# Kernel optimization log

Hardware: AMD Instinct MI355X
Metric: run time of the kernel (lower is better)

## Reference

```python
import jax, jax.numpy as jnp
import numpy as np

D_MODEL = 1024
N_HEADS = 16
HEAD_DIM = D_MODEL // N_HEADS


def setup_inputs() -> dict:
    key = jax.random.key(0)
    k1, k2, k3 = jax.random.split(key, 3)
    B, T, C = 4, 2048, D_MODEL
    x = jax.random.normal(k1, (B, T, C), dtype=jnp.float32)
    # torch Linear weight is (out,in); store as (in,out) so y = x @ W
    w_qkv = jax.random.normal(k2, (C, 3 * C), dtype=jnp.float32) * (1.0 / np.sqrt(C))
    w_proj = jax.random.normal(k3, (C, C), dtype=jnp.float32) * (1.0 / np.sqrt(C))
    return {"x": x, "w_qkv": w_qkv, "w_proj": w_proj}


def reference(x, w_qkv, w_proj):
    B, T, C = x.shape
    H, Dh = N_HEADS, HEAD_DIM
    qkv = x @ w_qkv                        # (B,T,3C)
    q, k, v = jnp.split(qkv, 3, axis=-1)
    def heads(t):
        return t.reshape(B, T, H, Dh).transpose(0, 2, 1, 3)  # (B,H,T,Dh)
    q, k, v = heads(q), heads(k), heads(v)
    scores = jnp.einsum('bhqd,bhkd->bhqk', q, k) / np.sqrt(Dh).astype(np.float32)
    causal = jnp.tril(jnp.ones((T, T), dtype=bool))
    scores = jnp.where(causal, scores, -jnp.inf)
    attn = jax.nn.softmax(scores, axis=-1)
    y = jnp.einsum('bhqk,bhkd->bhqd', attn, v)  # (B,H,T,Dh)
    y = y.transpose(0, 2, 1, 3).reshape(B, T, C)
    return y @ w_proj
```

## Files before the change

### kernel.cpp

```cpp
#include <hip/hip_runtime.h>

#define SEQ_T 2048
#define NBATCH 4
#define CDIM 1024
#define NHEAD 16
#define MROWS 8192
#define QKVC 3072

typedef unsigned short u16;
typedef __bf16 bf16x8 __attribute__((ext_vector_type(8)));
typedef float f32x4 __attribute__((ext_vector_type(4)));
typedef unsigned short u16x8 __attribute__((ext_vector_type(8)));
typedef unsigned uint32x4 __attribute__((ext_vector_type(4)));

__device__ __forceinline__ u16 f32_to_bf16(float f) {
  union { float f; unsigned int u; } v; v.f = f;
  unsigned int u = v.u;
  unsigned int r = ((u >> 16) & 1u) + 0x7fffu;
  return (u16)((u + r) >> 16);
}

__device__ __forceinline__ void gload_lds16(const u16* g, u16* l) {
  __builtin_amdgcn_global_load_lds(
      (const __attribute__((address_space(1))) void*)g,
      (__attribute__((address_space(3))) void*)l, 16, 0, 0);
}


__global__ __launch_bounds__(256) void cast_block_kernel(const float* __restrict__ in,
                                                         u16* __restrict__ out) {
  const int i = blockIdx.x * 256 + threadIdx.x;
  const int kg = i & 127;
  const int row = i >> 7;
  const float4 v0 = ((const float4*)in)[i * 2];
  const float4 v1 = ((const float4*)in)[i * 2 + 1];
  union { u16 u[8]; bf16x8 b; } o;
  o.u[0] = f32_to_bf16(v0.x); o.u[1] = f32_to_bf16(v0.y);
  o.u[2] = f32_to_bf16(v0.z); o.u[3] = f32_to_bf16(v0.w);
  o.u[4] = f32_to_bf16(v1.x); o.u[5] = f32_to_bf16(v1.y);
  o.u[6] = f32_to_bf16(v1.z); o.u[7] = f32_to_bf16(v1.w);
  const int tile = (row >> 4) * 32 + (kg >> 2);
  const int lane = (row & 15) + ((kg & 3) << 4);
  *(bf16x8*)(out + (size_t)tile * 512 + lane * 8) = o.b;
}

__global__ void transpose_cast_block_kernel(const float* __restrict__ in,
                                            u16* __restrict__ out) {
  __shared__ float tile[32][33];
  const int c0 = blockIdx.x * 32, r0 = blockIdx.y * 32;
  const int tx = threadIdx.x, ty = threadIdx.y;
  #pragma unroll
  for (int i = 0; i < 32; i += 8)
    tile[ty + i][tx] = in[(size_t)(r0 + ty + i) * QKVC + c0 + tx];
  __syncthreads();
  const int t = ty * 32 + tx;
  if (t < 128) {
    const int cc = t & 31, kgq = t >> 5;
    union { u16 u[8]; bf16x8 b; } o;
    #pragma unroll
    for (int j = 0; j < 8; ++j) o.u[j] = f32_to_bf16(tile[kgq * 8 + j][cc]);
    const int rowN = c0 + cc;
    const int tileI = (rowN >> 4) * 32 + (r0 >> 5);
    const int lane = (rowN & 15) + (kgq << 4);
    *(bf16x8*)(out + (size_t)tileI * 512 + lane * 8) = o.b;
  }
}

__global__ void transpose_cast_kernel(const float* __restrict__ in, u16* __restrict__ out,
                                      int R, int Cc) {
  __shared__ float tile[32][33];
  int c0 = blockIdx.x * 32, r0 = blockIdx.y * 32;
  int tx = threadIdx.x, ty = threadIdx.y;
  #pragma unroll
  for (int i = 0; i < 32; i += 8)
    tile[ty + i][tx] = in[(size_t)(r0 + ty + i) * Cc + c0 + tx];
  __syncthreads();
  #pragma unroll
  for (int i = 0; i < 32; i += 8)
    out[(size_t)(c0 + ty + i) * R + r0 + tx] = f32_to_bf16(tile[tx][ty + i]);
}

__global__ __launch_bounds__(256, 3)
void gemm1_kernel(const u16* __restrict__ Ab, const u16* __restrict__ Bb,
                  u16* __restrict__ Qb, u16* __restrict__ Kc, u16* __restrict__ Vc) {
  __shared__ u16 lds[24576];
  const int tid = threadIdx.x;
  const int lane = tid & 63, w = tid >> 6;
  const int wm = w >> 1, wn = w & 1;
  const int l15 = lane & 15, lhi = lane >> 4;
  const int row0 = blockIdx.x * 128, col0 = blockIdx.y * 128;
  const int rt0 = row0 >> 4, ct0 = col0 >> 4;

  const u16* aT = Ab + (size_t)(rt0 + w * 2) * 16384 + lane * 8;
  const u16* bT = Bb + (size_t)(ct0 + w * 2) * 16384 + lane * 8;

  f32x4 acc[4][4] = {};

#define SA(S) (lds + (S) * 4096)
#define SB(S) (lds + 12288 + (S) * 4096)
#define STAGE(KT, S)                                                            \
  {                                                                             \
    gload_lds16(aT + (size_t)(KT) * 512,         SA(S) + (w * 2) * 512);        \
    gload_lds16(aT + 16384 + (size_t)(KT) * 512, SA(S) + (w * 2 + 1) * 512);    \
    gload_lds16(bT + (size_t)(KT) * 512,         SB(S) + (w * 2) * 512);        \
    gload_lds16(bT + 16384 + (size_t)(KT) * 512, SB(S) + (w * 2 + 1) * 512);    \
  }
#define COMPUTE(S)                                                              \
  {                                                                             \
    bf16x8 af[4], bf[4];                                                        \
    _Pragma("unroll") for (int mi = 0; mi < 4; ++mi)                            \
      af[mi] = *(const bf16x8*)(SA(S) + (wm * 4 + mi) * 512 + lane * 8);        \
    _Pragma("unroll") for (int ni = 0; ni < 4; ++ni)                            \
      bf[ni] = *(const bf16x8*)(SB(S) + (wn * 4 + ni) * 512 + lane * 8);        \
    __builtin_amdgcn_s_setprio(1);                                              \
    _Pragma("unroll") for (int mi = 0; mi < 4; ++mi)                            \
      _Pragma("unroll") for (int ni = 0; ni < 4; ++ni)                          \
        acc[mi][ni] = __builtin_amdgcn_mfma_f32_16x16x32_bf16(af[mi], bf[ni],   \
                                                              acc[mi][ni], 0, 0, 0); \
    __builtin_amdgcn_s_setprio(0);                                              \
  }
#define WAITBAR4                                                                \
  asm volatile("s_waitcnt vmcnt(4)" ::: "memory");                              \
  __builtin_amdgcn_sched_barrier(0);                                            \
  __builtin_amdgcn_s_barrier();

  STAGE(0, 0);
  STAGE(1, 1);
  WAITBAR4;

  #pragma unroll 1
  for (int kt = 0; kt < 30; kt += 3) {
    STAGE(kt + 2, 2); COMPUTE(0); WAITBAR4;
    STAGE(kt + 3, 0); COMPUTE(1); WAITBAR4;
    STAGE(kt + 4, 1); COMPUTE(2); WAITBAR4;
  }
  COMPUTE(0);
  asm volatile("s_waitcnt vmcnt(0)" ::: "memory");
  __builtin_amdgcn_sched_barrier(0);
  __builtin_amdgcn_s_barrier();
  COMPUTE(1);
#undef STAGE
#undef COMPUTE
#undef WAITBAR4
#undef SA
#undef SB

  const int region = col0 >> 10;
  if (region == 0) {
    #pragma unroll
    for (int mt = 0; mt < 4; ++mt)
      #pragma unroll
      for (int nt = 0; nt < 4; ++nt)
        #pragma unroll
        for (int r = 0; r < 4; ++r) {
          const int rr = row0 + wm * 64 + mt * 16 + lhi * 4 + r;
          const int cc = col0 + wn * 64 + nt * 16 + l15;
          Qb[(size_t)rr * CDIM + cc] = f32_to_bf16(acc[mt][nt][r] * 0.18033688011f);
        }
  } else {
    __syncthreads();
    if (region == 1) {
      #pragma unroll
      for (int mt = 0; mt < 4; ++mt)
        #pragma unroll
        for (int nt = 0; nt < 4; ++nt)
          #pragma unroll
          for (int r = 0; r < 4; ++r) {
            const int sidx = (wn * 4 + wm * 2 + (mt >> 1)) * 2048
                           + ((mt & 1) * 2 + (nt >> 1)) * 512
                           + ((nt & 1) * 2 + (l15 >> 3)) * 128
                           + (lhi * 4 + r) * 8 + (l15 & 7);
            lds[sidx] = f32_to_bf16(acc[mt][nt][r]);
          }
    } else {
      #pragma unroll
      for (int mt = 0; mt < 4; ++mt)
        #pragma unroll
        for (int nt = 0; nt < 4; ++nt)
          #pragma unroll
          for (int r = 0; r < 4; ++r) {
            const int sidx = (wn * 4 + wm * 2 + (mt >> 1)) * 2048
                           + nt * 512
                           + ((mt & 1) * 2 + (lhi >> 1)) * 128
                           + l15 * 8 + (lhi & 1) * 4 + r;
            lds[sidx] = f32_to_bf16(acc[mt][nt][r]);
          }
    }
    __syncthreads();
    u16* dstB = (region == 1) ? Kc : Vc;
    const int bb = row0 >> 11;
    const int kv0b = (row0 & 2047) >> 5;
    const int hbase = (col0 & 1023) >> 6;
    #pragma unroll
    for (int hh = 0; hh < 2; ++hh) {
      u16* dst = dstB + (size_t)(bb * 16 + hbase + hh) * 131072 + (size_t)kv0b * 2048;
      const u16* src = lds + hh * 8192;
      #pragma unroll
      for (int c = 0; c < 4; ++c) {
        const int o = (c * 256 + tid) * 8;
        *(uint32x4*)(dst + o) = *(const uint32x4*)(src + o);
      }
    }
  }
}

__global__ __launch_bounds__(256, 3)
void gemm2_kernel(const u16* __restrict__ A, const u16* __restrict__ Bt,
                  float* __restrict__ C, int N, int K) {
  __shared__ u16 sA[3][4096];
  __shared__ u16 sB[3][4096];
  const int tid = threadIdx.x;
  const int lane = tid & 63, w = tid >> 6;
  const int wm = w >> 1, wn = w & 1;
  const int l15 = lane & 15, lhi = lane >> 4;
  const int row0 = blockIdx.x * 128, col0 = blockIdx.y * 128;

  const int oln  = ((lane & 3) - (lane >> 2)) & 3;
  const int srow = w * 32 + (lane >> 2);
  const u16* aS = A  + (size_t)(row0 + srow) * K + oln * 8;
  const u16* bS = Bt + (size_t)(col0 + srow) * K + oln * 8;
  const int stD = w * 1024;
  const int rdA = (wm * 64 + l15) * 32 + ((lhi + l15) & 3) * 8;
  const int rdB = (wn * 64 + l15) * 32 + ((lhi + l15) & 3) * 8;

  f32x4 acc[4][4] = {};

#define STAGE(KT, S)                                                            \
  {                                                                             \
    const size_t ko = (size_t)(KT) * 32;                                        \
    gload_lds16(aS + ko,          &sA[S][stD]);                                 \
    gload_lds16(aS + ko + 16 * K, &sA[S][stD + 512]);                           \
    gload_lds16(bS + ko,          &sB[S][stD]);                                 \
    gload_lds16(bS + ko + 16 * K, &sB[S][stD + 512]);                           \
  }
#define COMPUTE(S)                                                              \
  {                                                                             \
    bf16x8 af[4], bf[4];                                                        \
    _Pragma("unroll") for (int mi = 0; mi < 4; ++mi)                            \
      af[mi] = *(const bf16x8*)&sA[S][rdA + mi * 512];                          \
    _Pragma("unroll") for (int ni = 0; ni < 4; ++ni)                            \
      bf[ni] = *(const bf16x8*)&sB[S][rdB + ni * 512];                          \
    __builtin_amdgcn_s_setprio(1);                                              \
    _Pragma("unroll") for (int mi = 0; mi < 4; ++mi)                            \
      _Pragma("unroll") for (int ni = 0; ni < 4; ++ni)                          \
        acc[mi][ni] = __builtin_amdgcn_mfma_f32_16x16x32_bf16(af[mi], bf[ni],   \
                                                              acc[mi][ni], 0, 0, 0); \
    __builtin_amdgcn_s_setprio(0);                                              \
  }
#define WAITBAR4                                                                \
  asm volatile("s_waitcnt vmcnt(4)" ::: "memory");                              \
  __builtin_amdgcn_sched_barrier(0);                                            \
  __builtin_amdgcn_s_barrier();

  STAGE(0, 0);
  STAGE(1, 1);
  WAITBAR4;

  #pragma unroll 1
  for (int kt = 0; kt < 30; kt += 3) {
    STAGE(kt + 2, 2); COMPUTE(0); WAITBAR4;
    STAGE(kt + 3, 0); COMPUTE(1); WAITBAR4;
    STAGE(kt + 4, 1); COMPUTE(2); WAITBAR4;
  }
  COMPUTE(0);
  asm volatile("s_waitcnt vmcnt(0)" ::: "memory");
  __builtin_amdgcn_sched_barrier(0);
  __builtin_amdgcn_s_barrier();
  COMPUTE(1);
#undef STAGE
#undef COMPUTE
#undef WAITBAR4

  #pragma unroll
  for (int mt = 0; mt < 4; ++mt)
    #pragma unroll
    for (int nt = 0; nt < 4; ++nt)
      #pragma unroll
      for (int r = 0; r < 4; ++r) {
        const int rr = row0 + wm * 64 + mt * 16 + lhi * 4 + r;
        const int cc = col0 + wn * 64 + nt * 16 + l15;
        C[(size_t)rr * N + cc] = acc[mt][nt][r];
      }
}

template <bool DOMASK>
__device__ __forceinline__ void attn_step(const bf16x8 (&qf)[2],
                                          const bf16x8 (&kf)[2][2],
                                          const bf16x8 (&vb)[4],
                                          const bf16x8 ones,
                                          f32x4 (&acc)[4], f32x4& acc1,
                                          int l15, int lhi, int kv0, int qg) {
  f32x4 st[2];
  #pragma unroll
  for (int t = 0; t < 2; ++t) {
    f32x4 z = {0.f, 0.f, 0.f, 0.f};
    z = __builtin_amdgcn_mfma_f32_16x16x32_bf16(kf[t][0], qf[0], z, 0, 0, 0);
    z = __builtin_amdgcn_mfma_f32_16x16x32_bf16(kf[t][1], qf[1], z, 0, 0, 0);
    st[t] = z;
  }
  #pragma unroll
  for (int t = 0; t < 2; ++t)
    #pragma unroll
    for (int r = 0; r < 4; ++r) {
      float sv = st[t][r];
      if (DOMASK) {
        const int kvg = kv0 + t * 16 + lhi * 4 + r;
        sv = (kvg > qg) ? -__builtin_inff() : sv;
      }
      st[t][r] = exp2f(sv);
    }
  unsigned c00, c01, c10, c11;
  asm("v_cvt_pk_bf16_f32 %0, %1, %2" : "=v"(c00) : "v"(st[0][0]), "v"(st[0][1]));
  asm("v_cvt_pk_bf16_f32 %0, %1, %2" : "=v"(c01) : "v"(st[0][2]), "v"(st[0][3]));
  asm("v_cvt_pk_bf16_f32 %0, %1, %2" : "=v"(c10) : "v"(st[1][0]), "v"(st[1][1]));
  asm("v_cvt_pk_bf16_f32 %0, %1, %2" : "=v"(c11) : "v"(st[1][2]), "v"(st[1][3]));
  asm("v_permlane32_swap_b32 %0, %1" : "+v"(c00), "+v"(c10));
  asm("v_permlane32_swap_b32 %0, %1" : "+v"(c01), "+v"(c11));
  asm("v_permlane16_swap_b32 %0, %1" : "+v"(c00), "+v"(c10));
  asm("v_permlane16_swap_b32 %0, %1" : "+v"(c01), "+v"(c11));
  uint32x4 pw; pw[0] = c00; pw[1] = c01; pw[2] = c10; pw[3] = c11;
  const bf16x8 pa = __builtin_bit_cast(bf16x8, pw);
  #pragma unroll
  for (int d = 0; d < 4; ++d)
    acc[d] = __builtin_amdgcn_mfma_f32_16x16x32_bf16(pa, vb[d], acc[d], 0, 0, 0);
  acc1 = __builtin_amdgcn_mfma_f32_16x16x32_bf16(pa, ones, acc1, 0, 0, 0);
}

__global__ __launch_bounds__(256, 4) void attn_kernel(const u16* __restrict__ Qb,
                                                      const u16* __restrict__ Kc,
                                                      const u16* __restrict__ Vc,
                                                      u16* __restrict__ Y) {
  __shared__ u16 Kl[2][2048];
  __shared__ u16 Vl[2][2048];
  const int tid = threadIdx.x, lane = tid & 63, wid = tid >> 6;
  const int l15 = lane & 15, lhi = lane >> 4;
  const int id = blockIdx.x;
  const int xcd = id & 7, k = (id >> 3) & 15, hi3 = id >> 7;
  const int bh = hi3 * 8 + xcd;
  const int b = bh >> 4, h = bh & 15;
  const int pa = k * 4 + wid;
  const int qA0 = pa * 16, qB0 = (127 - pa) * 16;
  const int nchA = pa / 2 + 1, nchB = (127 - pa) / 2 + 1;
  const int ncmax = (127 - k * 4) / 2 + 1;
  const u16* Qp  = Qb + (size_t)b * SEQ_T * CDIM + h * 64;
  const u16* KcC = Kc + (size_t)bh * 131072;
  const u16* VcC = Vc + (size_t)bh * 131072;

  u16x8 ou;
  #pragma unroll
  for (int j = 0; j < 8; ++j) ou[j] = 0x3F80;
  const bf16x8 ones = __builtin_bit_cast(bf16x8, ou);

  gload_lds16(KcC + wid * 512 + lane * 8, &Kl[0][wid * 512]);
  gload_lds16(VcC + wid * 512 + lane * 8, &Vl[0][wid * 512]);

  bf16x8 qfA[2], qfB[2];
  #pragma unroll
  for (int i = 0; i < 2; ++i) {
    qfA[i] = *(const bf16x8*)(Qp + (size_t)(qA0 + l15) * CDIM + i * 32 + lhi * 8);
    qfB[i] = *(const bf16x8*)(Qp + (size_t)(qB0 + l15) * CDIM + i * 32 + lhi * 8);
  }
  const int qgA = qA0 + l15, qgB = qB0 + l15;

  f32x4 accA[4] = {}, accB[4] = {};
  f32x4 acc1A = {}, acc1B = {};

  __syncthreads();

  int cbuf = 0;
  for (int ic = 0; ic < ncmax; ++ic) {
    if (ic + 1 < ncmax) {
      const u16* kg = KcC + (size_t)(ic + 1) * 2048 + wid * 512 + lane * 8;
      const u16* vg = VcC + (size_t)(ic + 1) * 2048 + wid * 512 + lane * 8;
      gload_lds16(kg, &Kl[cbuf ^ 1][wid * 512]);
      gload_lds16(vg, &Vl[cbuf ^ 1][wid * 512]);
    }
    const u16* kb = &Kl[cbuf][0];
    const u16* vp = &Vl[cbuf][0];
    bf16x8 kf[2][2], vb[4];
    #pragma unroll
    for (int t = 0; t < 2; ++t)
      #pragma unroll
      for (int i = 0; i < 2; ++i)
        kf[t][i] = *(const bf16x8*)(kb + (t * 2 + i) * 512 + lane * 8);
    #pragma unroll
    for (int d = 0; d < 4; ++d)
      vb[d] = *(const bf16x8*)(vp + d * 512 + lane * 8);

    const int kv0 = ic * 32;
    if (ic < nchB) {
      if (ic == nchB - 1)
        attn_step<true>(qfB, kf, vb, ones, accB, acc1B, l15, lhi, kv0, qgB);
      else
        attn_step<false>(qfB, kf, vb, ones, accB, acc1B, l15, lhi, kv0, qgB);
    }
    if (ic < nchA) {
      if (ic == nchA - 1)
        attn_step<true>(qfA, kf, vb, ones, accA, acc1A, l15, lhi, kv0, qgA);
      else
        attn_step<false>(qfA, kf, vb, ones, accA, acc1A, l15, lhi, kv0, qgA);
    }
    __syncthreads();
    cbuf ^= 1;
  }

  u16* Yp = Y + (size_t)b * SEQ_T * CDIM + h * 64;
  #pragma unroll
  for (int r = 0; r < 4; ++r) {
    const float ivA = 1.0f / acc1A[r];
    const float ivB = 1.0f / acc1B[r];
    #pragma unroll
    for (int d = 0; d < 4; ++d) {
      Yp[(size_t)(qA0 + lhi * 4 + r) * CDIM + d * 16 + l15] = f32_to_bf16(accA[d][r] * ivA);
      Yp[(size_t)(qB0 + lhi * 4 + r) * CDIM + d * 16 + l15] = f32_to_bf16(accB[d][r] * ivB);
    }
  }
}

extern "C" void kernel_launch(void* const* d_in, const int* in_sizes, int n_in,
                              void* d_out, int out_size, void* d_ws, size_t ws_size,
                              hipStream_t stream) {
  const float* x      = (const float*)d_in[0];
  const float* w_qkv  = (const float*)d_in[1];
  const float* w_proj = (const float*)d_in[2];
  float* out = (float*)d_out;

  u16* Xb  = (u16*)d_ws;
  u16* Wqt = Xb  + (size_t)MROWS * CDIM;
  u16* Wpt = Wqt + (size_t)QKVC * CDIM;
  u16* Qb  = Wpt + (size_t)CDIM * CDIM;
  u16* Kc  = Qb  + (size_t)MROWS * CDIM;
  u16* Vc  = Kc  + (size_t)64 * 131072;
  u16* Yb  = Vc  + (size_t)64 * 131072;

  cast_block_kernel<<<MROWS * CDIM / 8 / 256, 256, 0, stream>>>(x, Xb);
  transpose_cast_block_kernel<<<dim3(QKVC / 32, CDIM / 32), dim3(32, 8), 0, stream>>>(w_qkv, Wqt);
  transpose_cast_kernel<<<dim3(CDIM / 32, CDIM / 32), dim3(32, 8), 0, stream>>>(w_proj, Wpt, CDIM, CDIM);

  gemm1_kernel<<<dim3(MROWS / 128, QKVC / 128), 256, 0, stream>>>(Xb, Wqt, Qb, Kc, Vc);

  attn_kernel<<<1024, 256, 0, stream>>>(Qb, Kc, Vc, Yb);

  gemm2_kernel<<<dim3(MROWS / 128, CDIM / 128), 256, 0, stream>>>(Yb, Wpt, out, CDIM, CDIM);
}
```

Baseline: 167.4 us.

## Write attention output in MFMA-tiled layout and double KV chunk per barrier

The attention kernel now writes Y directly in the 16x32 pre-tiled fragment layout, so gemm2 can load contiguous 512-element tiles with the same tiled addressing used by gemm1. The w_proj cast reuses the tiled transpose kernel. The attention loop also processes two 32-key chunks per LDS buffer, halving barriers and doubling prefetch size at the cost of more LDS. The intent is to cut swizzled LDS addressing in gemm2 and sync overhead in attention, though the scattered tiled bf16 stores from attention may be less coalesced.

Result: faster. 156.1 us (-6.7%).

```diff
diff --git a/kernel.cpp b/kernel.cpp
--- a/kernel.cpp
+++ b/kernel.cpp
@@ -45,13 +45,13 @@
 }
 
 __global__ void transpose_cast_block_kernel(const float* __restrict__ in,
-                                            u16* __restrict__ out) {
+                                            u16* __restrict__ out, int Cc) {
   __shared__ float tile[32][33];
   const int c0 = blockIdx.x * 32, r0 = blockIdx.y * 32;
   const int tx = threadIdx.x, ty = threadIdx.y;
   #pragma unroll
   for (int i = 0; i < 32; i += 8)
-    tile[ty + i][tx] = in[(size_t)(r0 + ty + i) * QKVC + c0 + tx];
+    tile[ty + i][tx] = in[(size_t)(r0 + ty + i) * Cc + c0 + tx];
   __syncthreads();
   const int t = ty * 32 + tx;
   if (t < 128) {
@@ -64,20 +64,6 @@
     const int lane = (rowN & 15) + (kgq << 4);
     *(bf16x8*)(out + (size_t)tileI * 512 + lane * 8) = o.b;
   }
-}
-
-__global__ void transpose_cast_kernel(const float* __restrict__ in, u16* __restrict__ out,
-                                      int R, int Cc) {
-  __shared__ float tile[32][33];
-  int c0 = blockIdx.x * 32, r0 = blockIdx.y * 32;
-  int tx = threadIdx.x, ty = threadIdx.y;
-  #pragma unroll
-  for (int i = 0; i < 32; i += 8)
-    tile[ty + i][tx] = in[(size_t)(r0 + ty + i) * Cc + c0 + tx];
-  __syncthreads();
-  #pragma unroll
-  for (int i = 0; i < 32; i += 8)
-    out[(size_t)(c0 + ty + i) * R + r0 + tx] = f32_to_bf16(tile[tx][ty + i]);
 }
 
 __global__ __launch_bounds__(256, 3)
@@ -205,41 +191,37 @@
 }
 
 __global__ __launch_bounds__(256, 3)
-void gemm2_kernel(const u16* __restrict__ A, const u16* __restrict__ Bt,
-                  float* __restrict__ C, int N, int K) {
-  __shared__ u16 sA[3][4096];
-  __shared__ u16 sB[3][4096];
+void gemm2_kernel(const u16* __restrict__ Ab, const u16* __restrict__ Bb,
+                  float* __restrict__ C) {
+  __shared__ u16 lds[24576];
   const int tid = threadIdx.x;
   const int lane = tid & 63, w = tid >> 6;
   const int wm = w >> 1, wn = w & 1;
   const int l15 = lane & 15, lhi = lane >> 4;
   const int row0 = blockIdx.x * 128, col0 = blockIdx.y * 128;
-
-  const int oln  = ((lane & 3) - (lane >> 2)) & 3;
-  const int srow = w * 32 + (lane >> 2);
-  const u16* aS = A  + (size_t)(row0 + srow) * K + oln * 8;
-  const u16* bS = Bt + (size_t)(col0 + srow) * K + oln * 8;
-  const int stD = w * 1024;
-  const int rdA = (wm * 64 + l15) * 32 + ((lhi + l15) & 3) * 8;
-  const int rdB = (wn * 64 + l15) * 32 + ((lhi + l15) & 3) * 8;
+  const int rt0 = row0 >> 4, ct0 = col0 >> 4;
+
+  const u16* aT = Ab + (size_t)(rt0 + w * 2) * 16384 + lane * 8;
+  const u16* bT = Bb + (size_t)(ct0 + w * 2) * 16384 + lane * 8;
 
   f32x4 acc[4][4] = {};
 
+#define SA(S) (lds + (S) * 4096)
+#define SB(S) (lds + 12288 + (S) * 4096)
 #define STAGE(KT, S)                                                            \
   {                                                                             \
-    const size_t ko = (size_t)(KT) * 32;                                        \
-    gload_lds16(aS + ko,          &sA[S][stD]);                                 \
-    gload_lds16(aS + ko + 16 * K, &sA[S][stD + 512]);                           \
-    gload_lds16(bS + ko,          &sB[S][stD]);                                 \
-    gload_lds16(bS + ko + 16 * K, &sB[S][stD + 512]);                           \
+    gload_lds16(aT + (size_t)(KT) * 512,         SA(S) + (w * 2) * 512);        \
+    gload_lds16(aT + 16384 + (size_t)(KT) * 512, SA(S) + (w * 2 + 1) * 512);    \
+    gload_lds16(bT + (size_t)(KT) * 512,         SB(S) + (w * 2) * 512);        \
+    gload_lds16(bT + 16384 + (size_t)(KT) * 512, SB(S) + (w * 2 + 1) * 512);    \
   }
 #define COMPUTE(S)                                                              \
   {                                                                             \
     bf16x8 af[4], bf[4];                                                        \
     _Pragma("unroll") for (int mi = 0; mi < 4; ++mi)                            \
-      af[mi] = *(const bf16x8*)&sA[S][rdA + mi * 512];                          \
+      af[mi] = *(const bf16x8*)(SA(S) + (wm * 4 + mi) * 512 + lane * 8);        \
     _Pragma("unroll") for (int ni = 0; ni < 4; ++ni)                            \
-      bf[ni] = *(const bf16x8*)&sB[S][rdB + ni * 512];                          \
+      bf[ni] = *(const bf16x8*)(SB(S) + (wn * 4 + ni) * 512 + lane * 8);        \
     __builtin_amdgcn_s_setprio(1);                                              \
     _Pragma("unroll") for (int mi = 0; mi < 4; ++mi)                            \
       _Pragma("unroll") for (int ni = 0; ni < 4; ++ni)                          \
@@ -270,6 +252,8 @@
 #undef STAGE
 #undef COMPUTE
 #undef WAITBAR4
+#undef SA
+#undef SB
 
   #pragma unroll
   for (int mt = 0; mt < 4; ++mt)
@@ -279,7 +263,7 @@
       for (int r = 0; r < 4; ++r) {
         const int rr = row0 + wm * 64 + mt * 16 + lhi * 4 + r;
         const int cc = col0 + wn * 64 + nt * 16 + l15;
-        C[(size_t)rr * N + cc] = acc[mt][nt][r];
+        C[(size_t)rr * CDIM + cc] = acc[mt][nt][r];
       }
 }
 
@@ -329,9 +313,9 @@
 __global__ __launch_bounds__(256, 4) void attn_kernel(const u16* __restrict__ Qb,
                                                       const u16* __restrict__ Kc,
                                                       const u16* __restrict__ Vc,
-                                                      u16* __restrict__ Y) {
-  __shared__ u16 Kl[2][2048];
-  __shared__ u16 Vl[2][2048];
+                                                      u16* __restrict__ Yb) {
+  __shared__ u16 Kl[2][4096];
+  __shared__ u16 Vl[2][4096];
   const int tid = threadIdx.x, lane = tid & 63, wid = tid >> 6;
   const int l15 = lane & 15, lhi = lane >> 4;
   const int id = blockIdx.x;
@@ -341,7 +325,7 @@
   const int pa = k * 4 + wid;
   const int qA0 = pa * 16, qB0 = (127 - pa) * 16;
   const int nchA = pa / 2 + 1, nchB = (127 - pa) / 2 + 1;
-  const int ncmax = (127 - k * 4) / 2 + 1;
+  const int nc2max = 32 - k;
   const u16* Qp  = Qb + (size_t)b * SEQ_T * CDIM + h * 64;
   const u16* KcC = Kc + (size_t)bh * 131072;
   const u16* VcC = Vc + (size_t)bh * 131072;
@@ -351,8 +335,10 @@
   for (int j = 0; j < 8; ++j) ou[j] = 0x3F80;
   const bf16x8 ones = __builtin_bit_cast(bf16x8, ou);
 
-  gload_lds16(KcC + wid * 512 + lane * 8, &Kl[0][wid * 512]);
-  gload_lds16(VcC + wid * 512 + lane * 8, &Vl[0][wid * 512]);
+  gload_lds16(KcC + wid * 512 + lane * 8,        &Kl[0][wid * 512]);
+  gload_lds16(KcC + 2048 + wid * 512 + lane * 8, &Kl[0][2048 + wid * 512]);
+  gload_lds16(VcC + wid * 512 + lane * 8,        &Vl[0][wid * 512]);
+  gload_lds16(VcC + 2048 + wid * 512 + lane * 8, &Vl[0][2048 + wid * 512]);
 
   bf16x8 qfA[2], qfB[2];
   #pragma unroll
@@ -368,51 +354,60 @@
   __syncthreads();
 
   int cbuf = 0;
-  for (int ic = 0; ic < ncmax; ++ic) {
-    if (ic + 1 < ncmax) {
-      const u16* kg = KcC + (size_t)(ic + 1) * 2048 + wid * 512 + lane * 8;
-      const u16* vg = VcC + (size_t)(ic + 1) * 2048 + wid * 512 + lane * 8;
-      gload_lds16(kg, &Kl[cbuf ^ 1][wid * 512]);
-      gload_lds16(vg, &Vl[cbuf ^ 1][wid * 512]);
-    }
-    const u16* kb = &Kl[cbuf][0];
-    const u16* vp = &Vl[cbuf][0];
-    bf16x8 kf[2][2], vb[4];
-    #pragma unroll
-    for (int t = 0; t < 2; ++t)
-      #pragma unroll
-      for (int i = 0; i < 2; ++i)
-        kf[t][i] = *(const bf16x8*)(kb + (t * 2 + i) * 512 + lane * 8);
-    #pragma unroll
-    for (int d = 0; d < 4; ++d)
-      vb[d] = *(const bf16x8*)(vp + d * 512 + lane * 8);
-
-    const int kv0 = ic * 32;
-    if (ic < nchB) {
-      if (ic == nchB - 1)
-        attn_step<true>(qfB, kf, vb, ones, accB, acc1B, l15, lhi, kv0, qgB);
-      else
-        attn_step<false>(qfB, kf, vb, ones, accB, acc1B, l15, lhi, kv0, qgB);
-    }
-    if (ic < nchA) {
-      if (ic == nchA - 1)
-        attn_step<true>(qfA, kf, vb, ones, accA, acc1A, l15, lhi, kv0, qgA);
-      else
-        attn_step<false>(qfA, kf, vb, ones, accA, acc1A, l15, lhi, kv0, qgA);
+  for (int ic2 = 0; ic2 < nc2max; ++ic2) {
+    if (ic2 + 1 < nc2max) {
+      const u16* kg = KcC + (size_t)(ic2 + 1) * 4096 + wid * 512 + lane * 8;
+      const u16* vg = VcC + (size_t)(ic2 + 1) * 4096 + wid * 512 + lane * 8;
+      gload_lds16(kg,        &Kl[cbuf ^ 1][wid * 512]);
+      gload_lds16(kg + 2048, &Kl[cbuf ^ 1][2048 + wid * 512]);
+      gload_lds16(vg,        &Vl[cbuf ^ 1][wid * 512]);
+      gload_lds16(vg + 2048, &Vl[cbuf ^ 1][2048 + wid * 512]);
+    }
+    #pragma unroll
+    for (int h2 = 0; h2 < 2; ++h2) {
+      const int c = ic2 * 2 + h2;
+      const u16* kb = &Kl[cbuf][h2 * 2048];
+      const u16* vp = &Vl[cbuf][h2 * 2048];
+      bf16x8 kf[2][2], vb[4];
+      #pragma unroll
+      for (int t = 0; t < 2; ++t)
+        #pragma unroll
+        for (int i = 0; i < 2; ++i)
+          kf[t][i] = *(const bf16x8*)(kb + (t * 2 + i) * 512 + lane * 8);
+      #pragma unroll
+      for (int d = 0; d < 4; ++d)
+        vb[d] = *(const bf16x8*)(vp + d * 512 + lane * 8);
+
+      const int kv0 = c * 32;
+      if (c < nchB) {
+        if (c == nchB - 1)
+          attn_step<true>(qfB, kf, vb, ones, accB, acc1B, l15, lhi, kv0, qgB);
+        else
+          attn_step<false>(qfB, kf, vb, ones, accB, acc1B, l15, lhi, kv0, qgB);
+      }
+      if (c < nchA) {
+        if (c == nchA - 1)
+          attn_step<true>(qfA, kf, vb, ones, accA, acc1A, l15, lhi, kv0, qgA);
+        else
+          attn_step<false>(qfA, kf, vb, ones, accA, acc1A, l15, lhi, kv0, qgA);
+      }
     }
     __syncthreads();
     cbuf ^= 1;
   }
 
-  u16* Yp = Y + (size_t)b * SEQ_T * CDIM + h * 64;
   #pragma unroll
   for (int r = 0; r < 4; ++r) {
     const float ivA = 1.0f / acc1A[r];
     const float ivB = 1.0f / acc1B[r];
+    const int rl = lhi * 4 + r;
     #pragma unroll
     for (int d = 0; d < 4; ++d) {
-      Yp[(size_t)(qA0 + lhi * 4 + r) * CDIM + d * 16 + l15] = f32_to_bf16(accA[d][r] * ivA);
-      Yp[(size_t)(qB0 + lhi * 4 + r) * CDIM + d * 16 + l15] = f32_to_bf16(accB[d][r] * ivB);
+      const int lofs = (rl + (((d * 2 + (l15 >> 3)) & 3) << 4)) * 8 + (l15 & 7);
+      Yb[((size_t)(b * 128 + pa)        * 32 + h * 2 + (d >> 1)) * 512 + lofs] =
+          f32_to_bf16(accA[d][r] * ivA);
+      Yb[((size_t)(b * 128 + (127 - pa)) * 32 + h * 2 + (d >> 1)) * 512 + lofs] =
+          f32_to_bf16(accB[d][r] * ivB);
     }
   }
 }
@@ -434,12 +429,12 @@
   u16* Yb  = Vc  + (size_t)64 * 131072;
 
   cast_block_kernel<<<MROWS * CDIM / 8 / 256, 256, 0, stream>>>(x, Xb);
-  transpose_cast_block_kernel<<<dim3(QKVC / 32, CDIM / 32), dim3(32, 8), 0, stream>>>(w_qkv, Wqt);
-  transpose_cast_kernel<<<dim3(CDIM / 32, CDIM / 32), dim3(32, 8), 0, stream>>>(w_proj, Wpt, CDIM, CDIM);
+  transpose_cast_block_kernel<<<dim3(QKVC / 32, CDIM / 32), dim3(32, 8), 0, stream>>>(w_qkv, Wqt, QKVC);
+  transpose_cast_block_kernel<<<dim3(CDIM / 32, CDIM / 32), dim3(32, 8), 0, stream>>>(w_proj, Wpt, CDIM);
 
   gemm1_kernel<<<dim3(MROWS / 128, QKVC / 128), 256, 0, stream>>>(Xb, Wqt, Qb, Kc, Vc);
 
   attn_kernel<<<1024, 256, 0, stream>>>(Qb, Kc, Vc, Yb);
 
-  gemm2_kernel<<<dim3(MROWS / 128, CDIM / 128), 256, 0, stream>>>(Yb, Wpt, out, CDIM, CDIM);
-}
+  gemm2_kernel<<<dim3(MROWS / 128, CDIM / 128), 256, 0, stream>>>(Yb, Wpt, out);
+}
```
